# Kernel optimization log

Hardware: AMD Instinct MI355X
Metric: run time of the kernel (lower is better)

Reference implementation:

```python
import jax, jax.numpy as jnp
import numpy as np

N = 50000      # nodes
E = 800000     # edges per meta-path
P = 3          # meta-paths
IN = 128       # in_size
OUT = 64       # out_size per head
H = 4          # heads
HID = 128      # semantic-attention hidden
NEG_SLOPE = 0.2


def setup_inputs() -> dict:
    key = jax.random.key(0)
    ks = jax.random.split(key, 8)
    h = jax.random.normal(ks[0], (N, IN), jnp.float32)
    edges = jax.random.randint(ks[1], (P, 2, E), 0, N, dtype=jnp.int32)  # [P, (src,dst), E]
    fc_w = jax.random.normal(ks[2], (P, IN, H * OUT), jnp.float32) * 0.05
    attn_l = jax.random.normal(ks[3], (P, H, OUT), jnp.float32) * 0.05
    attn_r = jax.random.normal(ks[4], (P, H, OUT), jnp.float32) * 0.05
    w1 = jax.random.normal(ks[5], (H * OUT, HID), jnp.float32) * 0.05
    b1 = jnp.zeros((HID,), jnp.float32)
    w2 = jax.random.normal(ks[6], (HID,), jnp.float32) * 0.05
    return {"h": h, "edges": edges, "fc_w": fc_w, "attn_l": attn_l,
            "attn_r": attn_r, "w1": w1, "b1": b1, "w2": w2}


def _gat(h, edge, fc_w, al, ar):
    # One GATConv (DGL semantics, eval mode: dropout off, no residual/bias).
    src, dst = edge[0], edge[1]
    feat = (h @ fc_w).reshape(N, H, OUT)                 # [N,H,D]
    el = jnp.einsum('nhd,hd->nh', feat, al)              # [N,H]
    er = jnp.einsum('nhd,hd->nh', feat, ar)
    e = jax.nn.leaky_relu(el[src] + er[dst], NEG_SLOPE)  # [E,H]
    # edge softmax over incoming edges of each dst node
    m = jax.ops.segment_max(e, dst, num_segments=N)      # [N,H]
    m = jnp.where(jnp.isfinite(m), m, 0.0)               # empty segments -> 0
    ex = jnp.exp(e - m[dst])
    s = jax.ops.segment_sum(ex, dst, num_segments=N)     # [N,H]
    alpha = ex / s[dst]                                  # [E,H]
    msg = feat[src] * alpha[:, :, None]                  # [E,H,D]
    rst = jax.ops.segment_sum(msg, dst, num_segments=N)  # [N,H,D]
    return jax.nn.elu(rst).reshape(N, H * OUT)


def reference(h, edges, fc_w, attn_l, attn_r, w1, b1, w2):
    # per-meta-path GAT embeddings -> [N, P, H*OUT]
    z = jnp.stack([_gat(h, edges[i], fc_w[i], attn_l[i], attn_r[i])
                   for i in range(P)], axis=1)
    # semantic attention: Linear -> tanh -> Linear(no bias) -> softmax over P
    w = jnp.tanh(z @ w1 + b1) @ w2                       # [N,P]
    beta = jax.nn.softmax(w, axis=1)[:, :, None]         # [N,P,1]
    return (beta * z).sum(axis=1)                        # [N, H*OUT]
```

## Files before the change

kernel.cpp:

```cpp
#include <hip/hip_runtime.h>
#include <hip/hip_bf16.h>
#include <hip/hip_fp16.h>

#define N_NODES 50000
#define N_EDGES 800000
#define N_PATHS 3
#define IN_F    128
#define HO      256
#define N_HEADS 4
#define HID     128

#define FEAT_RB       782
#define CNT_BLOCKS    2344
#define SCAT_BLOCKS   2344
#define PREP_T_BLOCKS 384
#define PREP_Z_BLOCKS 147
#define FEAT_ELEMS    ((size_t)N_NODES * HO)

typedef __bf16 bf16;
typedef __bf16 bf16x8 __attribute__((ext_vector_type(8)));
typedef float  f32x4  __attribute__((ext_vector_type(4)));
typedef unsigned short u16;

__global__ __launch_bounds__(256) void k_prep(const float* __restrict__ fc_w,
                                              bf16* __restrict__ fcwT,
                                              int* __restrict__ deg) {
    const int b = blockIdx.x;
    if (b < PREP_T_BLOCKS) {
        int g = b * 256 + threadIdx.x;
        int p = g >> 15, r = g & 32767;
        int col = r & 255, k = r >> 8;
        fcwT[(size_t)p * 32768 + col * IN_F + k] = (bf16)fc_w[(size_t)p * 32768 + k * HO + col];
    } else {
        int g = (b - PREP_T_BLOCKS) * 256 + threadIdx.x;
        if (g < (N_PATHS * N_NODES) / 4) {
            int4 zz = {0, 0, 0, 0};
            ((int4*)deg)[g] = zz;
        }
    }
}

__device__ __forceinline__ void count_role(int b, const int* __restrict__ edges,
                                           int* __restrict__ deg, u16* __restrict__ rank) {
    int gt = b * 256 + threadIdx.x;
    if (gt >= (N_PATHS * N_EDGES) / 4) return;
    int base = gt * 4;
    int p = base / N_EDGES, e = base - p * N_EDGES;
    const int* dstp = edges + (size_t)p * 2 * N_EDGES + N_EDGES;
    int4 d4 = *(const int4*)(dstp + e);
    int* dg = deg + p * N_NODES;
    u16 r0 = (u16)atomicAdd(&dg[d4.x], 1);
    u16 r1 = (u16)atomicAdd(&dg[d4.y], 1);
    u16 r2 = (u16)atomicAdd(&dg[d4.z], 1);
    u16 r3 = (u16)atomicAdd(&dg[d4.w], 1);
    ushort4 rr = {r0, r1, r2, r3};
    *(ushort4*)(rank + base) = rr;
}

__device__ __forceinline__ void feat_role(int rb, const float* __restrict__ h,
                                          const bf16* __restrict__ fcwT,
                                          const float* __restrict__ al,
                                          const float* __restrict__ ar,
                                          __half* __restrict__ featAll,
                                          float* __restrict__ elAll,
                                          float* __restrict__ erAll) {
    const int t = threadIdx.x, w = t >> 6, l = t & 63, lo = l & 15, hi = l >> 4;
    const int arow = rb * 64 + w * 16 + lo;
    const int crow = rb * 64 + w * 16 + hi * 4;

    bf16x8 afr[4];
    if (arow < N_NODES) {
        const float* hp = h + (size_t)arow * IN_F;
#pragma unroll
        for (int ks = 0; ks < 4; ++ks) {
            float4 f0 = *(const float4*)(hp + ks * 32 + hi * 8);
            float4 f1 = *(const float4*)(hp + ks * 32 + hi * 8 + 4);
            bf16x8 a;
            a[0]=(bf16)f0.x; a[1]=(bf16)f0.y; a[2]=(bf16)f0.z; a[3]=(bf16)f0.w;
            a[4]=(bf16)f1.x; a[5]=(bf16)f1.y; a[6]=(bf16)f1.z; a[7]=(bf16)f1.w;
            afr[ks] = a;
        }
    } else {
#pragma unroll
        for (int ks = 0; ks < 4; ++ks) { bf16x8 a = {}; afr[ks] = a; }
    }

    for (int p = 0; p < N_PATHS; ++p) {
        __half* feat = featAll + (size_t)p * FEAT_ELEMS;
        const float* alp = al + p * HO;
        const float* arp = ar + p * HO;
        float* elA = elAll + (size_t)p * N_NODES * 4;
        float* erA = erAll + (size_t)p * N_NODES * 4;
#pragma unroll
        for (int ch = 0; ch < 2; ++ch) {
            const bf16* W = fcwT + (size_t)p * 32768 + (size_t)ch * 128 * IN_F;
            f32x4 acc[8];
#pragma unroll
            for (int c = 0; c < 8; ++c) { f32x4 zz = {0.f,0.f,0.f,0.f}; acc[c] = zz; }
#pragma unroll
            for (int ctl = 0; ctl < 8; ++ctl) {
                const bf16* wp = W + (size_t)(ctl * 16 + lo) * IN_F + hi * 8;
                f32x4 a = acc[ctl];
#pragma unroll
                for (int ks = 0; ks < 4; ++ks)
                    a = __builtin_amdgcn_mfma_f32_16x16x32_bf16(afr[ks], *(const bf16x8*)(wp + ks * 32), a, 0, 0, 0);
                acc[ctl] = a;
            }
            float elP[2][4] = {{0}}, erP[2][4] = {{0}};
#pragma unroll
            for (int ctl = 0; ctl < 8; ++ctl) {
                const int gcol = ch * 128 + ctl * 16 + lo;
                const float av = alp[gcol], bv = arp[gcol];
                const int hl = ctl >> 2;
#pragma unroll
                for (int rr = 0; rr < 4; ++rr) {
                    float v = acc[ctl][rr];
                    elP[hl][rr] = fmaf(v, av, elP[hl][rr]);
                    erP[hl][rr] = fmaf(v, bv, erP[hl][rr]);
                    if (crow + rr < N_NODES)
                        feat[(size_t)(crow + rr) * HO + gcol] = __float2half(v);
                }
            }
#pragma unroll
            for (int hl = 0; hl < 2; ++hl)
#pragma unroll
                for (int rr = 0; rr < 4; ++rr) {
                    float v = elP[hl][rr], u = erP[hl][rr];
#pragma unroll
                    for (int m = 1; m <= 8; m <<= 1) {
                        v += __shfl_xor(v, m, 64);
                        u += __shfl_xor(u, m, 64);
                    }
                    elP[hl][rr] = v; erP[hl][rr] = u;
                }
            if (lo == 0) {
#pragma unroll
                for (int rr = 0; rr < 4; ++rr) {
                    if (crow + rr < N_NODES) {
                        *(float2*)&elA[(crow + rr) * 4 + ch * 2] = make_float2(elP[0][rr], elP[1][rr]);
                        *(float2*)&erA[(crow + rr) * 4 + ch * 2] = make_float2(erP[0][rr], erP[1][rr]);
                    }
                }
            }
        }
    }
}

__global__ __launch_bounds__(256, 4) void k_cf(const int* __restrict__ edges,
                                               int* __restrict__ deg,
                                               u16* __restrict__ rank,
                                               const float* __restrict__ h,
                                               const bf16* __restrict__ fcwT,
                                               const float* __restrict__ al,
                                               const float* __restrict__ ar,
                                               __half* __restrict__ featAll,
                                               float* __restrict__ elAll,
                                               float* __restrict__ erAll) {
    const int bid = blockIdx.x;
    if (bid < CNT_BLOCKS)
        count_role(bid, edges, deg, rank);
    else
        feat_role(bid - CNT_BLOCKS, h, fcwT, al, ar, featAll, elAll, erAll);
}

__global__ __launch_bounds__(1024) void k_scan(const int* __restrict__ deg,
                                               int* __restrict__ rowptr) {
    __shared__ int part[1024];
    const int p = blockIdx.x;
    const int* dg = deg + p * N_NODES;
    int* rp = rowptr + p * (N_NODES + 1);

    const int tid = threadIdx.x;
    const int CH = (N_NODES + 1023) / 1024;
    const int start = tid * CH;
    int s = 0;
    for (int i = 0; i < CH; ++i) { int idx = start + i; if (idx < N_NODES) s += dg[idx]; }
    part[tid] = s;
    __syncthreads();
    for (int off = 1; off < 1024; off <<= 1) {
        int v = (tid >= off) ? part[tid - off] : 0;
        __syncthreads();
        part[tid] += v;
        __syncthreads();
    }
    int excl = (tid == 0) ? 0 : part[tid - 1];
    for (int i = 0; i < CH; ++i) {
        int idx = start + i;
        if (idx < N_NODES) { rp[idx] = excl; excl += dg[idx]; }
    }
    if (tid == 1023) rp[N_NODES] = N_EDGES;
}

__global__ __launch_bounds__(256) void k_scatter(const int* __restrict__ edges,
                                                 const u16* __restrict__ rank,
                                                 const int* __restrict__ rowptr,
                                                 u16* __restrict__ csr) {
    int gt = blockIdx.x * 256 + threadIdx.x;
    if (gt >= (N_PATHS * N_EDGES) / 4) return;
    int base = gt * 4;
    int p = base / N_EDGES, e = base - p * N_EDGES;
    const int* ep = edges + (size_t)p * 2 * N_EDGES;
    int4 s4 = *(const int4*)(ep + e);
    int4 d4 = *(const int4*)(ep + N_EDGES + e);
    ushort4 r4 = *(const ushort4*)(rank + base);
    const int* rp = rowptr + p * (N_NODES + 1);
    u16* c = csr + (size_t)p * N_EDGES;
    c[rp[d4.x] + r4.x] = (u16)s4.x;
    c[rp[d4.y] + r4.y] = (u16)s4.y;
    c[rp[d4.z] + r4.z] = (u16)s4.z;
    c[rp[d4.w] + r4.w] = (u16)s4.w;
}

__global__ __launch_bounds__(256) void k_gather3(const u16* __restrict__ csrAll,
                                                 const int* __restrict__ rowptrAll,
                                                 const float4* __restrict__ elAll,
                                                 const float4* __restrict__ erAll,
                                                 const __half* __restrict__ featAll,
                                                 bf16* __restrict__ z) {
    __shared__ int     off_lds[4][64];
    __shared__ __half2 a_lds[4][64][4];
    const int pb = blockIdx.x;
    const int p  = pb / (N_NODES / 4);
    const int nb = pb - p * (N_NODES / 4);
    const u16*    csr    = csrAll + (size_t)p * N_EDGES;
    const int*    rowptr = rowptrAll + p * (N_NODES + 1);
    const float4* el4    = elAll + (size_t)p * N_NODES;
    const float4* er4    = erAll + (size_t)p * N_NODES;
    const __half* feat   = featAll + (size_t)p * FEAT_ELEMS;

    const int wid = threadIdx.x >> 6, l = threadIdx.x & 63;
    const int n = nb * 4 + wid;
    const int half = l >> 5, c = l & 31, hh = c >> 3;

    const int b0 = rowptr[n], b1 = rowptr[n + 1];
    const float4 er_n = er4[n];

    __half2 acc0 = __float2half2_rn(0.f), acc1 = acc0, acc2 = acc0, acc3 = acc0;
    float4 den = {0.f, 0.f, 0.f, 0.f};

    for (int base = b0; base < b1; base += 64) {
        const int cnt = min(64, b1 - base);
        if (l < cnt) {
            int sv = csr[base + l];
            off_lds[wid][l] = sv * HO;
            float4 e = el4[sv];
            float vx = e.x + er_n.x, vy = e.y + er_n.y,
                  vz = e.z + er_n.z, vw = e.w + er_n.w;
            vx = (vx >= 0.f) ? vx : 0.2f * vx;
            vy = (vy >= 0.f) ? vy : 0.2f * vy;
            vz = (vz >= 0.f) ? vz : 0.2f * vz;
            vw = (vw >= 0.f) ? vw : 0.2f * vw;
            float ex = __expf(vx), ey = __expf(vy), ez = __expf(vz), ew = __expf(vw);
            den.x += ex; den.y += ey; den.z += ez; den.w += ew;
            a_lds[wid][l][0] = __float2half2_rn(ex);
            a_lds[wid][l][1] = __float2half2_rn(ey);
            a_lds[wid][l][2] = __float2half2_rn(ez);
            a_lds[wid][l][3] = __float2half2_rn(ew);
        }
        for (int i2 = 0; i2 < cnt; i2 += 2) {
            const int e = i2 + half;
            if (e < cnt) {
                const int off = off_lds[wid][e];
                const __half2 a2 = a_lds[wid][e][hh];
                const uint4 u = *(const uint4*)(feat + off + c * 8);
                acc0 = __hfma2(__builtin_bit_cast(__half2, u.x), a2, acc0);
                acc1 = __hfma2(__builtin_bit_cast(__half2, u.y), a2, acc1);
                acc2 = __hfma2(__builtin_bit_cast(__half2, u.z), a2, acc2);
                acc3 = __hfma2(__builtin_bit_cast(__half2, u.w), a2, acc3);
            }
        }
    }

    float s[8];
    { float2 f0 = __half22float2(acc0), f1 = __half22float2(acc1),
             f2 = __half22float2(acc2), f3 = __half22float2(acc3);
      s[0]=f0.x; s[1]=f0.y; s[2]=f1.x; s[3]=f1.y; s[4]=f2.x; s[5]=f2.y; s[6]=f3.x; s[7]=f3.y; }
#pragma unroll
    for (int j = 0; j < 8; ++j) s[j] += __shfl_xor(s[j], 32, 64);
#pragma unroll
    for (int off = 32; off; off >>= 1) {
        den.x += __shfl_xor(den.x, off, 64);
        den.y += __shfl_xor(den.y, off, 64);
        den.z += __shfl_xor(den.z, off, 64);
        den.w += __shfl_xor(den.w, off, 64);
    }
    const float d = (hh == 0) ? den.x : (hh == 1) ? den.y : (hh == 2) ? den.z : den.w;
    const float inv = (d > 0.f) ? 1.f / d : 0.f;
    if (half == 0) {
        bf16x8 ov;
#pragma unroll
        for (int j = 0; j < 8; ++j) {
            float v = s[j] * inv;
            v = (v > 0.f) ? v : expm1f(v);
            ov[j] = (bf16)v;
        }
        *(bf16x8*)(z + (size_t)n * (N_PATHS * HO) + p * HO + c * 8) = ov;
    }
}

__global__ __launch_bounds__(256) void k_semout(const bf16* __restrict__ z,
                                                const float* __restrict__ w1,
                                                const float* __restrict__ b1,
                                                const float* __restrict__ w2,
                                                float* __restrict__ out) {
    __shared__ bf16  zs[48 * 264];
    __shared__ float psem[4][48];
    __shared__ float betas[16][4];

    const int t = threadIdx.x, w = t >> 6, l = t & 63;
    const int lo = l & 15, hi = l >> 4;
    const int n0 = blockIdx.x * 16;

    bf16x8 bfr[2][8];
#pragma unroll
    for (int ct = 0; ct < 2; ++ct) {
        const int j = (2 * w + ct) * 16 + lo;
#pragma unroll
        for (int s = 0; s < 8; ++s) {
            const int k0 = s * 32 + hi * 8;
            bf16x8 b;
#pragma unroll
            for (int i = 0; i < 8; ++i) b[i] = (bf16)w1[(k0 + i) * HID + j];
            bfr[ct][s] = b;
        }
    }

    const uint4* zg4 = (const uint4*)(z + (size_t)n0 * (N_PATHS * HO));
    for (int i = t; i < 1536; i += 256) {
        uint4 v = zg4[i];
        int r = i >> 5, cin = (i & 31) * 8;
        *(uint4*)&zs[r * 264 + cin] = v;
    }
    __syncthreads();

    f32x4 acc[2][3];
#pragma unroll
    for (int ct = 0; ct < 2; ++ct)
#pragma unroll
        for (int m = 0; m < 3; ++m) { f32x4 zz = {0.f,0.f,0.f,0.f}; acc[ct][m] = zz; }

    for (int s = 0; s < 8; ++s) {
#pragma unroll
        for (int m = 0; m < 3; ++m) {
            bf16x8 a = *(const bf16x8*)&zs[(m * 16 + lo) * 264 + s * 32 + hi * 8];
            acc[0][m] = __builtin_amdgcn_mfma_f32_16x16x32_bf16(a, bfr[0][s], acc[0][m], 0, 0, 0);
            acc[1][m] = __builtin_amdgcn_mfma_f32_16x16x32_bf16(a, bfr[1][s], acc[1][m], 0, 0, 0);
        }
    }

    const int j0 = (2 * w + 0) * 16 + lo;
    const int j1 = (2 * w + 1) * 16 + lo;
    const float b1_0 = b1[j0], w2_0 = w2[j0];
    const float b1_1 = b1[j1], w2_1 = w2[j1];
#pragma unroll
    for (int m = 0; m < 3; ++m) {
#pragma unroll
        for (int r = 0; r < 4; ++r) {
            float tt = tanhf(acc[0][m][r] + b1_0) * w2_0
                     + tanhf(acc[1][m][r] + b1_1) * w2_1;
            tt += __shfl_xor(tt, 1, 64);
            tt += __shfl_xor(tt, 2, 64);
            tt += __shfl_xor(tt, 4, 64);
            tt += __shfl_xor(tt, 8, 64);
            if (lo == 0) psem[w][m * 16 + hi * 4 + r] = tt;
        }
    }
    __syncthreads();
    if (t < 48) psem[0][t] = psem[0][t] + psem[1][t] + psem[2][t] + psem[3][t];
    __syncthreads();
    if (t < 16) {
        float a0 = psem[0][3 * t], a1 = psem[0][3 * t + 1], a2 = psem[0][3 * t + 2];
        float mx = fmaxf(a0, fmaxf(a1, a2));
        float e0 = __expf(a0 - mx), e1 = __expf(a1 - mx), e2 = __expf(a2 - mx);
        float is = 1.f / (e0 + e1 + e2);
        betas[t][0] = e0 * is; betas[t][1] = e1 * is; betas[t][2] = e2 * is;
    }
    __syncthreads();
    for (int i = 0; i < 16; ++i) {
        float bb0 = betas[i][0], bb1 = betas[i][1], bb2 = betas[i][2];
        float o = bb0 * (float)zs[(3 * i + 0) * 264 + t]
                + bb1 * (float)zs[(3 * i + 1) * 264 + t]
                + bb2 * (float)zs[(3 * i + 2) * 264 + t];
        out[(size_t)(n0 + i) * HO + t] = o;
    }
}

static inline size_t align256(size_t x) { return (x + 255) & ~(size_t)255; }

extern "C" void kernel_launch(void* const* d_in, const int* in_sizes, int n_in,
                              void* d_out, int out_size, void* d_ws, size_t ws_size,
                              hipStream_t stream) {
    const float* h     = (const float*)d_in[0];
    const int*   edges = (const int*)d_in[1];
    const float* fc_w  = (const float*)d_in[2];
    const float* al    = (const float*)d_in[3];
    const float* ar    = (const float*)d_in[4];
    const float* w1    = (const float*)d_in[5];
    const float* b1    = (const float*)d_in[6];
    const float* w2    = (const float*)d_in[7];
    float* out = (float*)d_out;

    char* base = (char*)d_ws;
    size_t off = 0;
    auto carve = [&](size_t bytes) -> char* {
        char* p = base + off; off = align256(off + bytes); return p;
    };
    bf16*   zbuf   = (bf16*)carve((size_t)N_NODES * N_PATHS * HO * 2);
    __half* feat   = (__half*)carve((size_t)N_PATHS * FEAT_ELEMS * 2);
    bf16*   fcwT   = (bf16*)carve((size_t)N_PATHS * IN_F * HO * 2);
    float*  el     = (float*)carve((size_t)N_PATHS * N_NODES * 4 * 4);
    float*  er     = (float*)carve((size_t)N_PATHS * N_NODES * 4 * 4);
    int*    deg    = (int*)carve((size_t)N_PATHS * N_NODES * 4);
    int*    rowptr = (int*)carve((size_t)N_PATHS * (N_NODES + 1) * 4);
    u16*    rank   = (u16*)carve((size_t)N_PATHS * N_EDGES * 2);
    u16*    csr    = (u16*)carve((size_t)N_PATHS * N_EDGES * 2);
    (void)ws_size; (void)in_sizes; (void)n_in; (void)out_size;

    k_prep<<<PREP_T_BLOCKS + PREP_Z_BLOCKS, 256, 0, stream>>>(fc_w, fcwT, deg);
    k_cf<<<CNT_BLOCKS + FEAT_RB, 256, 0, stream>>>(
        edges, deg, rank, h, fcwT, al, ar, feat, el, er);
    k_scan<<<N_PATHS, 1024, 0, stream>>>(deg, rowptr);
    k_scatter<<<SCAT_BLOCKS, 256, 0, stream>>>(edges, rank, rowptr, csr);
    k_gather3<<<N_PATHS * (N_NODES / 4), 256, 0, stream>>>(
        csr, rowptr, (const float4*)el, (const float4*)er, feat, zbuf);
    k_semout<<<N_NODES / 16, 256, 0, stream>>>(zbuf, w1, b1, w2, out);
}
```

Baseline: 558.3 us.

## Build CSR via per-block shared-memory histograms instead of global atomics

Replaces global atomic degree counting with per-block LDS histograms that pack four 8-bit node counts per word, storing local ranks as bytes. A new pass turns the per-block counts into per-block prefix offsets and degrees. The scatter then combines rowptr, block offset and local rank, and runs fused with the feature GEMM instead of the counting step. This aims to cut contended global atomics and rank traffic. The cost is extra histogram memory traffic, an added launch, and a reliance on each per-block count staying below 256.

```diff
diff --git a/kernel.cpp b/kernel.cpp
--- a/kernel.cpp
+++ b/kernel.cpp
@@ -10,51 +10,126 @@
 #define N_HEADS 4
 #define HID     128
 
-#define FEAT_RB       782
-#define CNT_BLOCKS    2344
-#define SCAT_BLOCKS   2344
-#define PREP_T_BLOCKS 384
-#define PREP_Z_BLOCKS 147
-#define FEAT_ELEMS    ((size_t)N_NODES * HO)
+#define BLK_PER_PATH 32
+#define EDGES_PER_HB 25000
+#define HIST_BLOCKS  (N_PATHS * BLK_PER_PATH)
+#define NPACK        12500
+#define FEAT_RB      782
+#define SCAT_BLOCKS  2344
+#define FEAT_ELEMS   ((size_t)N_NODES * HO)
 
 typedef __bf16 bf16;
 typedef __bf16 bf16x8 __attribute__((ext_vector_type(8)));
 typedef float  f32x4  __attribute__((ext_vector_type(4)));
 typedef unsigned short u16;
+typedef unsigned char  u8;
+typedef unsigned int   u32;
 
 __global__ __launch_bounds__(256) void k_prep(const float* __restrict__ fc_w,
-                                              bf16* __restrict__ fcwT,
+                                              bf16* __restrict__ fcwT) {
+    int g = blockIdx.x * 256 + threadIdx.x;
+    int p = g >> 15, r = g & 32767;
+    int col = r & 255, k = r >> 8;
+    fcwT[(size_t)p * 32768 + col * IN_F + k] = (bf16)fc_w[(size_t)p * 32768 + k * HO + col];
+}
+
+__global__ __launch_bounds__(256) void k_hist(const int* __restrict__ edges,
+                                              u32* __restrict__ cnt32,
+                                              u8* __restrict__ lrank) {
+    __shared__ u32 hist[NPACK];
+    const int b = blockIdx.x;
+    const int p = b / BLK_PER_PATH, blk = b - p * BLK_PER_PATH;
+    const int t = threadIdx.x;
+    for (int i = t; i < NPACK; i += 256) hist[i] = 0;
+    __syncthreads();
+
+    const int* dstp = edges + (size_t)p * 2 * N_EDGES + N_EDGES + blk * EDGES_PER_HB;
+    u8* lr = lrank + (size_t)p * N_EDGES + blk * EDGES_PER_HB;
+    for (int q = t; q < EDGES_PER_HB / 4; q += 256) {
+        int4 d4 = ((const int4*)dstp)[q];
+        u32 o0 = atomicAdd(&hist[d4.x >> 2], 1u << ((d4.x & 3) * 8));
+        u32 o1 = atomicAdd(&hist[d4.y >> 2], 1u << ((d4.y & 3) * 8));
+        u32 o2 = atomicAdd(&hist[d4.z >> 2], 1u << ((d4.z & 3) * 8));
+        u32 o3 = atomicAdd(&hist[d4.w >> 2], 1u << ((d4.w & 3) * 8));
+        uchar4 r4;
+        r4.x = (u8)(o0 >> ((d4.x & 3) * 8));
+        r4.y = (u8)(o1 >> ((d4.y & 3) * 8));
+        r4.z = (u8)(o2 >> ((d4.z & 3) * 8));
+        r4.w = (u8)(o3 >> ((d4.w & 3) * 8));
+        ((uchar4*)lr)[q] = r4;
+    }
+    __syncthreads();
+    u32* out = cnt32 + (size_t)b * NPACK;
+    for (int i = t; i < NPACK; i += 256) out[i] = hist[i];
+}
+
+__global__ __launch_bounds__(256) void k_base(u32* __restrict__ cnt32,
                                               int* __restrict__ deg) {
-    const int b = blockIdx.x;
-    if (b < PREP_T_BLOCKS) {
-        int g = b * 256 + threadIdx.x;
-        int p = g >> 15, r = g & 32767;
-        int col = r & 255, k = r >> 8;
-        fcwT[(size_t)p * 32768 + col * IN_F + k] = (bf16)fc_w[(size_t)p * 32768 + k * HO + col];
-    } else {
-        int g = (b - PREP_T_BLOCKS) * 256 + threadIdx.x;
-        if (g < (N_PATHS * N_NODES) / 4) {
-            int4 zz = {0, 0, 0, 0};
-            ((int4*)deg)[g] = zz;
-        }
-    }
-}
-
-__device__ __forceinline__ void count_role(int b, const int* __restrict__ edges,
-                                           int* __restrict__ deg, u16* __restrict__ rank) {
+    int g = blockIdx.x * 256 + threadIdx.x;
+    if (g >= N_PATHS * NPACK) return;
+    int p = g / NPACK, q = g - p * NPACK;
+    u32 s0 = 0, s1 = 0, s2 = 0, s3 = 0;
+#pragma unroll
+    for (int blk = 0; blk < BLK_PER_PATH; ++blk) {
+        size_t idx = (size_t)(p * BLK_PER_PATH + blk) * NPACK + q;
+        u32 c = cnt32[idx];
+        cnt32[idx] = s0 | (s1 << 8) | (s2 << 16) | (s3 << 24);
+        s0 += c & 0xff; s1 += (c >> 8) & 0xff; s2 += (c >> 16) & 0xff; s3 += c >> 24;
+    }
+    int4 d4 = {(int)s0, (int)s1, (int)s2, (int)s3};
+    *(int4*)(deg + (size_t)p * N_NODES + 4 * q) = d4;
+}
+
+__global__ __launch_bounds__(1024) void k_scan(const int* __restrict__ deg,
+                                               int* __restrict__ rowptr) {
+    __shared__ int part[1024];
+    const int p = blockIdx.x;
+    const int* dg = deg + p * N_NODES;
+    int* rp = rowptr + p * (N_NODES + 1);
+
+    const int tid = threadIdx.x;
+    const int CH = (N_NODES + 1023) / 1024;
+    const int start = tid * CH;
+    int s = 0;
+    for (int i = 0; i < CH; ++i) { int idx = start + i; if (idx < N_NODES) s += dg[idx]; }
+    part[tid] = s;
+    __syncthreads();
+    for (int off = 1; off < 1024; off <<= 1) {
+        int v = (tid >= off) ? part[tid - off] : 0;
+        __syncthreads();
+        part[tid] += v;
+        __syncthreads();
+    }
+    int excl = (tid == 0) ? 0 : part[tid - 1];
+    for (int i = 0; i < CH; ++i) {
+        int idx = start + i;
+        if (idx < N_NODES) { rp[idx] = excl; excl += dg[idx]; }
+    }
+    if (tid == 1023) rp[N_NODES] = N_EDGES;
+}
+
+__device__ __forceinline__ void scatter_role(int b, const int* __restrict__ edges,
+                                             const u8* __restrict__ lrank,
+                                             const u32* __restrict__ cnt32,
+                                             const int* __restrict__ rowptr,
+                                             u16* __restrict__ csr) {
     int gt = b * 256 + threadIdx.x;
     if (gt >= (N_PATHS * N_EDGES) / 4) return;
     int base = gt * 4;
     int p = base / N_EDGES, e = base - p * N_EDGES;
-    const int* dstp = edges + (size_t)p * 2 * N_EDGES + N_EDGES;
-    int4 d4 = *(const int4*)(dstp + e);
-    int* dg = deg + p * N_NODES;
-    u16 r0 = (u16)atomicAdd(&dg[d4.x], 1);
-    u16 r1 = (u16)atomicAdd(&dg[d4.y], 1);
-    u16 r2 = (u16)atomicAdd(&dg[d4.z], 1);
-    u16 r3 = (u16)atomicAdd(&dg[d4.w], 1);
-    ushort4 rr = {r0, r1, r2, r3};
-    *(ushort4*)(rank + base) = rr;
+    const int blk = e / EDGES_PER_HB;
+    const int* ep = edges + (size_t)p * 2 * N_EDGES;
+    int4 s4 = *(const int4*)(ep + e);
+    int4 d4 = *(const int4*)(ep + N_EDGES + e);
+    uchar4 r4 = *(const uchar4*)(lrank + base);
+    const int* rp = rowptr + p * (N_NODES + 1);
+    const u32* bb = cnt32 + (size_t)(p * BLK_PER_PATH + blk) * NPACK;
+    u16* c = csr + (size_t)p * N_EDGES;
+    int p0 = rp[d4.x] + ((bb[d4.x >> 2] >> ((d4.x & 3) * 8)) & 0xff) + r4.x;
+    int p1 = rp[d4.y] + ((bb[d4.y >> 2] >> ((d4.y & 3) * 8)) & 0xff) + r4.y;
+    int p2 = rp[d4.z] + ((bb[d4.z >> 2] >> ((d4.z & 3) * 8)) & 0xff) + r4.z;
+    int p3 = rp[d4.w] + ((bb[d4.w >> 2] >> ((d4.w & 3) * 8)) & 0xff) + r4.w;
+    c[p0] = (u16)s4.x; c[p1] = (u16)s4.y; c[p2] = (u16)s4.z; c[p3] = (u16)s4.w;
 }
 
 __device__ __forceinline__ void feat_role(int rb, const float* __restrict__ h,
@@ -146,9 +221,11 @@
     }
 }
 
-__global__ __launch_bounds__(256, 4) void k_cf(const int* __restrict__ edges,
-                                               int* __restrict__ deg,
-                                               u16* __restrict__ rank,
+__global__ __launch_bounds__(256, 4) void k_fs(const int* __restrict__ edges,
+                                               const u8* __restrict__ lrank,
+                                               const u32* __restrict__ cnt32,
+                                               const int* __restrict__ rowptr,
+                                               u16* __restrict__ csr,
                                                const float* __restrict__ h,
                                                const bf16* __restrict__ fcwT,
                                                const float* __restrict__ al,
@@ -157,58 +234,10 @@
                                                float* __restrict__ elAll,
                                                float* __restrict__ erAll) {
     const int bid = blockIdx.x;
-    if (bid < CNT_BLOCKS)
-        count_role(bid, edges, deg, rank);
+    if (bid < SCAT_BLOCKS)
+        scatter_role(bid, edges, lrank, cnt32, rowptr, csr);
     else
-        feat_role(bid - CNT_BLOCKS, h, fcwT, al, ar, featAll, elAll, erAll);
-}
-
-__global__ __launch_bounds__(1024) void k_scan(const int* __restrict__ deg,
-                                               int* __restrict__ rowptr) {
-    __shared__ int part[1024];
-    const int p = blockIdx.x;
-    const int* dg = deg + p * N_NODES;
-    int* rp = rowptr + p * (N_NODES + 1);
-
-    const int tid = threadIdx.x;
-    const int CH = (N_NODES + 1023) / 1024;
-    const int start = tid * CH;
-    int s = 0;
-    for (int i = 0; i < CH; ++i) { int idx = start + i; if (idx < N_NODES) s += dg[idx]; }
-    part[tid] = s;
-    __syncthreads();
-    for (int off = 1; off < 1024; off <<= 1) {
-        int v = (tid >= off) ? part[tid - off] : 0;
-        __syncthreads();
-        part[tid] += v;
-        __syncthreads();
-    }
-    int excl = (tid == 0) ? 0 : part[tid - 1];
-    for (int i = 0; i < CH; ++i) {
-        int idx = start + i;
-        if (idx < N_NODES) { rp[idx] = excl; excl += dg[idx]; }
-    }
-    if (tid == 1023) rp[N_NODES] = N_EDGES;
-}
-
-__global__ __launch_bounds__(256) void k_scatter(const int* __restrict__ edges,
-                                                 const u16* __restrict__ rank,
-                                                 const int* __restrict__ rowptr,
-                                                 u16* __restrict__ csr) {
-    int gt = blockIdx.x * 256 + threadIdx.x;
-    if (gt >= (N_PATHS * N_EDGES) / 4) return;
-    int base = gt * 4;
-    int p = base / N_EDGES, e = base - p * N_EDGES;
-    const int* ep = edges + (size_t)p * 2 * N_EDGES;
-    int4 s4 = *(const int4*)(ep + e);
-    int4 d4 = *(const int4*)(ep + N_EDGES + e);
-    ushort4 r4 = *(const ushort4*)(rank + base);
-    const int* rp = rowptr + p * (N_NODES + 1);
-    u16* c = csr + (size_t)p * N_EDGES;
-    c[rp[d4.x] + r4.x] = (u16)s4.x;
-    c[rp[d4.y] + r4.y] = (u16)s4.y;
-    c[rp[d4.z] + r4.z] = (u16)s4.z;
-    c[rp[d4.w] + r4.w] = (u16)s4.w;
+        feat_role(bid - SCAT_BLOCKS, h, fcwT, al, ar, featAll, elAll, erAll);
 }
 
 __global__ __launch_bounds__(256) void k_gather3(const u16* __restrict__ csrAll,
@@ -412,15 +441,17 @@
     float*  er     = (float*)carve((size_t)N_PATHS * N_NODES * 4 * 4);
     int*    deg    = (int*)carve((size_t)N_PATHS * N_NODES * 4);
     int*    rowptr = (int*)carve((size_t)N_PATHS * (N_NODES + 1) * 4);
-    u16*    rank   = (u16*)carve((size_t)N_PATHS * N_EDGES * 2);
+    u8*     lrank  = (u8*)carve((size_t)N_PATHS * N_EDGES);
     u16*    csr    = (u16*)carve((size_t)N_PATHS * N_EDGES * 2);
+    u32*    cnt32  = (u32*)carve((size_t)HIST_BLOCKS * NPACK * 4);
     (void)ws_size; (void)in_sizes; (void)n_in; (void)out_size;
 
-    k_prep<<<PREP_T_BLOCKS + PREP_Z_BLOCKS, 256, 0, stream>>>(fc_w, fcwT, deg);
-    k_cf<<<CNT_BLOCKS + FEAT_RB, 256, 0, stream>>>(
-        edges, deg, rank, h, fcwT, al, ar, feat, el, er);
+    k_prep<<<384, 256, 0, stream>>>(fc_w, fcwT);
+    k_hist<<<HIST_BLOCKS, 256, 0, stream>>>(edges, cnt32, lrank);
+    k_base<<<(N_PATHS * NPACK + 255) / 256, 256, 0, stream>>>(cnt32, deg);
     k_scan<<<N_PATHS, 1024, 0, stream>>>(deg, rowptr);
-    k_scatter<<<SCAT_BLOCKS, 256, 0, stream>>>(edges, rank, rowptr, csr);
+    k_fs<<<SCAT_BLOCKS + FEAT_RB, 256, 0, stream>>>(
+        edges, lrank, cnt32, rowptr, csr, h, fcwT, al, ar, feat, el, er);
     k_gather3<<<N_PATHS * (N_NODES / 4), 256, 0, stream>>>(
         csr, rowptr, (const float4*)el, (const float4*)er, feat, zbuf);
     k_semout<<<N_NODES / 16, 256, 0, stream>>>(zbuf, w1, b1, w2, out);
```

Measured after the change: 492.3 us. -11.8%, faster.
